# Kernel optimization log

Hardware: AMD Instinct MI355X
Metric: run time of the kernel (lower is better)

Reference implementation:

```python
import jax, jax.numpy as jnp
import numpy as np


def setup_inputs() -> dict:
    key = jax.random.key(0)
    ks = jax.random.split(key, 6)
    n_sess, n_trials = 4096, 2048
    chose_left = jax.random.bernoulli(ks[0], 0.5, (n_sess, n_trials)).astype(jnp.float32)
    chose_right = 1.0 - chose_left
    outcome = jax.random.bernoulli(ks[1], 0.5, (n_sess, n_trials)).astype(jnp.float32)
    inp = jnp.stack([chose_left, chose_right, outcome], axis=-1)  # (B, T, 3)
    return {
        "input": inp,
        # raw (pre-sigmoid) alpha logits, as stored by torch parametrize
        "a_same_rew": jax.random.normal(ks[2], (1,), jnp.float32),
        "a_same_unrew": jax.random.normal(ks[3], (1,), jnp.float32),
        "a_diff_rew": jax.random.normal(ks[4], (1,), jnp.float32),
        "a_diff_unrew": jax.random.normal(ks[5], (1,), jnp.float32),
        "k_same_rew": jnp.ones((1,), jnp.float32),
        "k_same_unrew": jnp.zeros((1,), jnp.float32),
        "k_diff_rew": jnp.ones((1,), jnp.float32),
        "k_diff_unrew": jnp.zeros((1,), jnp.float32),
    }


def _qvalue_scan(inp, a_sr, a_su, a_dr, a_du, k_sr, k_su, k_dr, k_du):
    # alphas via UnitConstraint (sigmoid of raw logit)
    alphas = jax.nn.sigmoid(jnp.concatenate([a_sr, a_su, a_dr, a_du]))  # (4,)
    ksr, ksu, kdr, kdu = k_sr[0], k_su[0], k_dr[0], k_du[0]
    B = inp.shape[0]

    def step(v, x_t):  # v: (B,2), x_t: (B,3)
        cl, cr, o = x_t[:, 0], x_t[:, 1], x_t[:, 2]
        no = 1.0 - o

        def side(same, other, vcol):
            d = jnp.stack([same * o * (ksr - vcol),
                           same * no * (ksu - vcol),
                           other * o * (kdr - vcol),
                           other * no * (kdu - vcol)], axis=1)  # (B,4)
            return d.sum(axis=1), d @ alphas  # diff, delta per side

        diff_l, del_l = side(cl, cr, v[:, 0])
        diff_r, del_r = side(cr, cl, v[:, 1])
        delta = jnp.stack([del_l, del_r], axis=1)  # (B,2)
        diff = jnp.stack([diff_l, diff_r], axis=1)
        new_v = v + delta
        return new_v, (new_v, diff, delta)

    v0 = jnp.zeros((B, 2), inp.dtype)
    _, (out_v, out_diff, out_delta) = jax.lax.scan(step, v0, jnp.swapaxes(inp, 0, 1))
    # (T,B,2) -> (B,T,2)
    tr = lambda a: jnp.swapaxes(a, 0, 1)
    return tr(out_v), tr(out_diff), tr(out_delta)


def reference(input, a_same_rew, a_same_unrew, a_diff_rew, a_diff_unrew,
              k_same_rew, k_same_unrew, k_diff_rew, k_diff_unrew):
    return _qvalue_scan(input, a_same_rew, a_same_unrew, a_diff_rew, a_diff_unrew,
                        k_same_rew, k_same_unrew, k_diff_rew, k_diff_unrew)
```

## Files before the change

kernel.cpp:

```cpp
#include <hip/hip_runtime.h>
#include <math.h>

#define B_SESS 4096
#define T_TR   2048
#define NCH    256
#define CL     8
#define NG     32
#define GL     8


__global__ __launch_bounds__(256) void qvalue_kernel(
    const float* __restrict__ inp,
    const float* __restrict__ p_asr, const float* __restrict__ p_asu,
    const float* __restrict__ p_adr, const float* __restrict__ p_adu,
    const float* __restrict__ p_ksr, const float* __restrict__ p_ksu,
    const float* __restrict__ p_kdr, const float* __restrict__ p_kdu,
    float* __restrict__ out)
{
    __shared__ float sIn[T_TR * 3];
    __shared__ float sA[NCH * 2];
    __shared__ float sB[NCH * 2];
    __shared__ float sGA[NG * 2];
    __shared__ float sGB[NG * 2];
    __shared__ float sGV[NG * 2];
    __shared__ float sV[NCH * 2];

    const int s   = blockIdx.x;
    const int tid = threadIdx.x;

    const float4* in4 = (const float4*)(inp + (size_t)s * (T_TR * 3));
    #pragma unroll
    for (int k = 0; k < 6; ++k) {
        int p4 = k * 256 + tid;
        float4 w = in4[p4];
        float vals[4] = {w.x, w.y, w.z, w.w};
        #pragma unroll
        for (int e = 0; e < 4; ++e) {
            int p = p4 * 4 + e;
            int t = p / 3;
            int c = p - t * 3;
            sIn[((t & (CL - 1)) * NCH + (t >> 3)) * 3 + c] = vals[e];
        }
    }

    float a0 = 1.f / (1.f + expf(-p_asr[0]));
    float a1 = 1.f / (1.f + expf(-p_asu[0]));
    float a2 = 1.f / (1.f + expf(-p_adr[0]));
    float a3 = 1.f / (1.f + expf(-p_adu[0]));
    float k0 = p_ksr[0], k1 = p_ksu[0], k2 = p_kdr[0], k3 = p_kdu[0];
    float b0 = a0 * k0, b1 = a1 * k1, b2 = a2 * k2, b3 = a3 * k3;

    __syncthreads();

    {
        const int j = tid;
        float AL = 1.f, BL = 0.f, AR = 1.f, BR = 0.f;
        #pragma unroll
        for (int l = 0; l < CL; ++l) {
            int base = (l * NCH + j) * 3;
            float cl = sIn[base], cr = sIn[base + 1], o = sIn[base + 2];
            float no = 1.f - o;
            float m0 = cl * o, m1 = cl * no, m2 = cr * o, m3 = cr * no;
            float coefL = a0 * m0 + a1 * m1 + a2 * m2 + a3 * m3;
            float rhsL  = b0 * m0 + b1 * m1 + b2 * m2 + b3 * m3;
            float coefR = a0 * m2 + a1 * m3 + a2 * m0 + a3 * m1;
            float rhsR  = b0 * m2 + b1 * m3 + b2 * m0 + b3 * m1;
            float gL = 1.f - coefL, gR = 1.f - coefR;
            AL = AL * gL;  BL = BL * gL + rhsL;
            AR = AR * gR;  BR = BR * gR + rhsR;
        }
        sA[j * 2 + 0] = AL;  sB[j * 2 + 0] = BL;
        sA[j * 2 + 1] = AR;  sB[j * 2 + 1] = BR;
    }
    __syncthreads();

    if (tid < NG * 2) {
        int g = tid >> 1, sd = tid & 1;
        float A = 1.f, Bc = 0.f;
        #pragma unroll
        for (int q = 0; q < GL; ++q) {
            int j = g * GL + q;
            float a = sA[j * 2 + sd], b = sB[j * 2 + sd];
            A = a * A;  Bc = a * Bc + b;
        }
        sGA[g * 2 + sd] = A;  sGB[g * 2 + sd] = Bc;
    }
    __syncthreads();

    if (tid < 2) {
        int sd = tid;
        float v = 0.f;
        #pragma unroll
        for (int g = 0; g < NG; ++g) {
            sGV[g * 2 + sd] = v;
            v = sGA[g * 2 + sd] * v + sGB[g * 2 + sd];
        }
    }
    __syncthreads();

    if (tid < NG * 2) {
        int g = tid >> 1, sd = tid & 1;
        float v = sGV[g * 2 + sd];
        #pragma unroll
        for (int q = 0; q < GL; ++q) {
            int j = g * GL + q;
            sV[j * 2 + sd] = v;
            v = sA[j * 2 + sd] * v + sB[j * 2 + sd];
        }
    }
    __syncthreads();

    {
        const int j = tid;
        float vL = sV[j * 2 + 0], vR = sV[j * 2 + 1];
        float vb[2 * CL], fb[2 * CL], db[2 * CL];
        #pragma unroll
        for (int l = 0; l < CL; ++l) {
            int base = (l * NCH + j) * 3;
            float cl = sIn[base], cr = sIn[base + 1], o = sIn[base + 2];
            float no = 1.f - o;
            float m0 = cl * o, m1 = cl * no, m2 = cr * o, m3 = cr * no;
            float coefL = a0 * m0 + a1 * m1 + a2 * m2 + a3 * m3;
            float rhsL  = b0 * m0 + b1 * m1 + b2 * m2 + b3 * m3;
            float coefR = a0 * m2 + a1 * m3 + a2 * m0 + a3 * m1;
            float rhsR  = b0 * m2 + b1 * m3 + b2 * m0 + b3 * m1;
            float s0  = m0 + m1 + m2 + m3;
            float s1L = k0 * m0 + k1 * m1 + k2 * m2 + k3 * m3;
            float s1R = k0 * m2 + k1 * m3 + k2 * m0 + k3 * m1;
            float dL = rhsL - coefL * vL;
            float dR = rhsR - coefR * vR;
            float fL = s1L - s0 * vL;
            float fR = s1R - s0 * vR;
            vL += dL;  vR += dR;
            vb[2 * l] = vL;  vb[2 * l + 1] = vR;
            fb[2 * l] = fL;  fb[2 * l + 1] = fR;
            db[2 * l] = dL;  db[2 * l + 1] = dR;
        }
        const size_t N2   = (size_t)B_SESS * T_TR * 2;
        const size_t boff = (size_t)s * (T_TR * 2) + (size_t)j * (CL * 2);
        float4* ov = (float4*)(out + boff);
        float4* of = (float4*)(out + N2 + boff);
        float4* od = (float4*)(out + 2 * N2 + boff);
        #pragma unroll
        for (int q = 0; q < (2 * CL) / 4; ++q) {
            ov[q] = make_float4(vb[4 * q], vb[4 * q + 1], vb[4 * q + 2], vb[4 * q + 3]);
            of[q] = make_float4(fb[4 * q], fb[4 * q + 1], fb[4 * q + 2], fb[4 * q + 3]);
            od[q] = make_float4(db[4 * q], db[4 * q + 1], db[4 * q + 2], db[4 * q + 3]);
        }
    }
}

extern "C" void kernel_launch(void* const* d_in, const int* in_sizes, int n_in,
                              void* d_out, int out_size, void* d_ws, size_t ws_size,
                              hipStream_t stream) {
    (void)in_sizes; (void)n_in; (void)out_size; (void)d_ws; (void)ws_size;
    qvalue_kernel<<<B_SESS, 256, 0, stream>>>(
        (const float*)d_in[0],
        (const float*)d_in[1], (const float*)d_in[2],
        (const float*)d_in[3], (const float*)d_in[4],
        (const float*)d_in[5], (const float*)d_in[6],
        (const float*)d_in[7], (const float*)d_in[8],
        (float*)d_out);
}
```

Baseline: 314.3 us.

## Use wavefront shuffle scan and LDS-staged coalesced output stores

Replaces the three-level shared-memory scan over chunk transforms with an in-wavefront shuffle-up scan plus a small cross-wave combine, removing several serial phases and barriers in which only a few threads were active. Outputs are staged through the input LDS buffer so each wave writes contiguous float4 rows instead of per-thread strided 64-byte segments. It also adds a min-blocks-per-CU launch bound. The cost is extra barriers and LDS round-trips for the three output arrays.

```diff
diff --git a/kernel.cpp b/kernel.cpp
--- a/kernel.cpp
+++ b/kernel.cpp
@@ -5,11 +5,9 @@
 #define T_TR   2048
 #define NCH    256
 #define CL     8
-#define NG     32
-#define GL     8
 
 
-__global__ __launch_bounds__(256) void qvalue_kernel(
+__global__ __launch_bounds__(256, 4) void qvalue_kernel(
     const float* __restrict__ inp,
     const float* __restrict__ p_asr, const float* __restrict__ p_asu,
     const float* __restrict__ p_adr, const float* __restrict__ p_adu,
@@ -18,22 +16,19 @@
     float* __restrict__ out)
 {
     __shared__ float sIn[T_TR * 3];
-    __shared__ float sA[NCH * 2];
-    __shared__ float sB[NCH * 2];
-    __shared__ float sGA[NG * 2];
-    __shared__ float sGB[NG * 2];
-    __shared__ float sGV[NG * 2];
-    __shared__ float sV[NCH * 2];
+    __shared__ float sWT[4 * 4];
 
-    const int s   = blockIdx.x;
-    const int tid = threadIdx.x;
+    const int s    = blockIdx.x;
+    const int tid  = threadIdx.x;
+    const int lane = tid & 63;
+    const int w    = tid >> 6;
 
     const float4* in4 = (const float4*)(inp + (size_t)s * (T_TR * 3));
     #pragma unroll
     for (int k = 0; k < 6; ++k) {
         int p4 = k * 256 + tid;
-        float4 w = in4[p4];
-        float vals[4] = {w.x, w.y, w.z, w.w};
+        float4 wv = in4[p4];
+        float vals[4] = {wv.x, wv.y, wv.z, wv.w};
         #pragma unroll
         for (int e = 0; e < 4; ++e) {
             int p = p4 * 4 + e;
@@ -52,102 +47,112 @@
 
     __syncthreads();
 
-    {
-        const int j = tid;
-        float AL = 1.f, BL = 0.f, AR = 1.f, BR = 0.f;
-        #pragma unroll
-        for (int l = 0; l < CL; ++l) {
-            int base = (l * NCH + j) * 3;
-            float cl = sIn[base], cr = sIn[base + 1], o = sIn[base + 2];
-            float no = 1.f - o;
-            float m0 = cl * o, m1 = cl * no, m2 = cr * o, m3 = cr * no;
-            float coefL = a0 * m0 + a1 * m1 + a2 * m2 + a3 * m3;
-            float rhsL  = b0 * m0 + b1 * m1 + b2 * m2 + b3 * m3;
-            float coefR = a0 * m2 + a1 * m3 + a2 * m0 + a3 * m1;
-            float rhsR  = b0 * m2 + b1 * m3 + b2 * m0 + b3 * m1;
-            float gL = 1.f - coefL, gR = 1.f - coefR;
-            AL = AL * gL;  BL = BL * gL + rhsL;
-            AR = AR * gR;  BR = BR * gR + rhsR;
+    float AL = 1.f, BL = 0.f, AR = 1.f, BR = 0.f;
+    #pragma unroll
+    for (int l = 0; l < CL; ++l) {
+        int base = (l * NCH + tid) * 3;
+        float cl = sIn[base], cr = sIn[base + 1], o = sIn[base + 2];
+        float no = 1.f - o;
+        float m0 = cl * o, m1 = cl * no, m2 = cr * o, m3 = cr * no;
+        float coefL = a0 * m0 + a1 * m1 + a2 * m2 + a3 * m3;
+        float rhsL  = b0 * m0 + b1 * m1 + b2 * m2 + b3 * m3;
+        float coefR = a0 * m2 + a1 * m3 + a2 * m0 + a3 * m1;
+        float rhsR  = b0 * m2 + b1 * m3 + b2 * m0 + b3 * m1;
+        float gL = 1.f - coefL, gR = 1.f - coefR;
+        AL = AL * gL;  BL = BL * gL + rhsL;
+        AR = AR * gR;  BR = BR * gR + rhsR;
+    }
+
+    #pragma unroll
+    for (int d = 1; d < 64; d <<= 1) {
+        float tAL = __shfl_up(AL, d, 64);
+        float tBL = __shfl_up(BL, d, 64);
+        float tAR = __shfl_up(AR, d, 64);
+        float tBR = __shfl_up(BR, d, 64);
+        if (lane >= d) {
+            BL = AL * tBL + BL;  AL = AL * tAL;
+            BR = AR * tBR + BR;  AR = AR * tAR;
         }
-        sA[j * 2 + 0] = AL;  sB[j * 2 + 0] = BL;
-        sA[j * 2 + 1] = AR;  sB[j * 2 + 1] = BR;
     }
+    if (lane == 63) {
+        sWT[w * 4 + 0] = AL;  sWT[w * 4 + 1] = BL;
+        sWT[w * 4 + 2] = AR;  sWT[w * 4 + 3] = BR;
+    }
+    float eAL = __shfl_up(AL, 1, 64), eBL = __shfl_up(BL, 1, 64);
+    float eAR = __shfl_up(AR, 1, 64), eBR = __shfl_up(BR, 1, 64);
+    if (lane == 0) { eAL = 1.f; eBL = 0.f; eAR = 1.f; eBR = 0.f; }
+
     __syncthreads();
 
-    if (tid < NG * 2) {
-        int g = tid >> 1, sd = tid & 1;
-        float A = 1.f, Bc = 0.f;
-        #pragma unroll
-        for (int q = 0; q < GL; ++q) {
-            int j = g * GL + q;
-            float a = sA[j * 2 + sd], b = sB[j * 2 + sd];
-            A = a * A;  Bc = a * Bc + b;
-        }
-        sGA[g * 2 + sd] = A;  sGB[g * 2 + sd] = Bc;
+    float vbL = 0.f, vbR = 0.f;
+    for (int ww = 0; ww < w; ++ww) {
+        vbL = sWT[ww * 4 + 0] * vbL + sWT[ww * 4 + 1];
+        vbR = sWT[ww * 4 + 2] * vbR + sWT[ww * 4 + 3];
     }
+    float vL = eAL * vbL + eBL;
+    float vR = eAR * vbR + eBR;
+
+    float vb[2 * CL], fb[2 * CL], db[2 * CL];
+    #pragma unroll
+    for (int l = 0; l < CL; ++l) {
+        int base = (l * NCH + tid) * 3;
+        float cl = sIn[base], cr = sIn[base + 1], o = sIn[base + 2];
+        float no = 1.f - o;
+        float m0 = cl * o, m1 = cl * no, m2 = cr * o, m3 = cr * no;
+        float coefL = a0 * m0 + a1 * m1 + a2 * m2 + a3 * m3;
+        float rhsL  = b0 * m0 + b1 * m1 + b2 * m2 + b3 * m3;
+        float coefR = a0 * m2 + a1 * m3 + a2 * m0 + a3 * m1;
+        float rhsR  = b0 * m2 + b1 * m3 + b2 * m0 + b3 * m1;
+        float s0  = m0 + m1 + m2 + m3;
+        float s1L = k0 * m0 + k1 * m1 + k2 * m2 + k3 * m3;
+        float s1R = k0 * m2 + k1 * m3 + k2 * m0 + k3 * m1;
+        float dL = rhsL - coefL * vL;
+        float dR = rhsR - coefR * vR;
+        float fL = s1L - s0 * vL;
+        float fR = s1R - s0 * vR;
+        vL += dL;  vR += dR;
+        vb[2 * l] = vL;  vb[2 * l + 1] = vR;
+        fb[2 * l] = fL;  fb[2 * l + 1] = fR;
+        db[2 * l] = dL;  db[2 * l + 1] = dR;
+    }
+
+    __syncthreads();
+    float* rb = sIn + (w << 10);
+    const size_t N2    = (size_t)B_SESS * T_TR * 2;
+    const size_t gbase = (size_t)s * (T_TR * 2) + ((size_t)w << 10);
+
+    float4* ov = (float4*)(out + gbase);
+    float4* of = (float4*)(out + N2 + gbase);
+    float4* od = (float4*)(out + 2 * N2 + gbase);
+
+    #pragma unroll
+    for (int q = 0; q < 4; ++q)
+        ((float4*)(rb + lane * 16))[q] =
+            make_float4(vb[4 * q], vb[4 * q + 1], vb[4 * q + 2], vb[4 * q + 3]);
+    __syncthreads();
+    #pragma unroll
+    for (int q = 0; q < 4; ++q)
+        ov[q * 64 + lane] = ((const float4*)rb)[q * 64 + lane];
     __syncthreads();
 
-    if (tid < 2) {
-        int sd = tid;
-        float v = 0.f;
-        #pragma unroll
-        for (int g = 0; g < NG; ++g) {
-            sGV[g * 2 + sd] = v;
-            v = sGA[g * 2 + sd] * v + sGB[g * 2 + sd];
-        }
-    }
+    #pragma unroll
+    for (int q = 0; q < 4; ++q)
+        ((float4*)(rb + lane * 16))[q] =
+            make_float4(fb[4 * q], fb[4 * q + 1], fb[4 * q + 2], fb[4 * q + 3]);
+    __syncthreads();
+    #pragma unroll
+    for (int q = 0; q < 4; ++q)
+        of[q * 64 + lane] = ((const float4*)rb)[q * 64 + lane];
     __syncthreads();
 
-    if (tid < NG * 2) {
-        int g = tid >> 1, sd = tid & 1;
-        float v = sGV[g * 2 + sd];
-        #pragma unroll
-        for (int q = 0; q < GL; ++q) {
-            int j = g * GL + q;
-            sV[j * 2 + sd] = v;
-            v = sA[j * 2 + sd] * v + sB[j * 2 + sd];
-        }
-    }
+    #pragma unroll
+    for (int q = 0; q < 4; ++q)
+        ((float4*)(rb + lane * 16))[q] =
+            make_float4(db[4 * q], db[4 * q + 1], db[4 * q + 2], db[4 * q + 3]);
     __syncthreads();
-
-    {
-        const int j = tid;
-        float vL = sV[j * 2 + 0], vR = sV[j * 2 + 1];
-        float vb[2 * CL], fb[2 * CL], db[2 * CL];
-        #pragma unroll
-        for (int l = 0; l < CL; ++l) {
-            int base = (l * NCH + j) * 3;
-            float cl = sIn[base], cr = sIn[base + 1], o = sIn[base + 2];
-            float no = 1.f - o;
-            float m0 = cl * o, m1 = cl * no, m2 = cr * o, m3 = cr * no;
-            float coefL = a0 * m0 + a1 * m1 + a2 * m2 + a3 * m3;
-            float rhsL  = b0 * m0 + b1 * m1 + b2 * m2 + b3 * m3;
-            float coefR = a0 * m2 + a1 * m3 + a2 * m0 + a3 * m1;
-            float rhsR  = b0 * m2 + b1 * m3 + b2 * m0 + b3 * m1;
-            float s0  = m0 + m1 + m2 + m3;
-            float s1L = k0 * m0 + k1 * m1 + k2 * m2 + k3 * m3;
-            float s1R = k0 * m2 + k1 * m3 + k2 * m0 + k3 * m1;
-            float dL = rhsL - coefL * vL;
-            float dR = rhsR - coefR * vR;
-            float fL = s1L - s0 * vL;
-            float fR = s1R - s0 * vR;
-            vL += dL;  vR += dR;
-            vb[2 * l] = vL;  vb[2 * l + 1] = vR;
-            fb[2 * l] = fL;  fb[2 * l + 1] = fR;
-            db[2 * l] = dL;  db[2 * l + 1] = dR;
-        }
-        const size_t N2   = (size_t)B_SESS * T_TR * 2;
-        const size_t boff = (size_t)s * (T_TR * 2) + (size_t)j * (CL * 2);
-        float4* ov = (float4*)(out + boff);
-        float4* of = (float4*)(out + N2 + boff);
-        float4* od = (float4*)(out + 2 * N2 + boff);
-        #pragma unroll
-        for (int q = 0; q < (2 * CL) / 4; ++q) {
-            ov[q] = make_float4(vb[4 * q], vb[4 * q + 1], vb[4 * q + 2], vb[4 * q + 3]);
-            of[q] = make_float4(fb[4 * q], fb[4 * q + 1], fb[4 * q + 2], fb[4 * q + 3]);
-            od[q] = make_float4(db[4 * q], db[4 * q + 1], db[4 * q + 2], db[4 * q + 3]);
-        }
-    }
+    #pragma unroll
+    for (int q = 0; q < 4; ++q)
+        od[q * 64 + lane] = ((const float4*)rb)[q * 64 + lane];
 }
 
 extern "C" void kernel_launch(void* const* d_in, const int* in_sizes, int n_in,
```

New measurement: 296.8 us. 1.06x faster.
